# Optimization experiments

Measured on AMD Instinct MI355X. Metric: run time of the kernel, lower is better.

Reference implementation:

```python
import math
import jax, jax.numpy as jnp
import numpy as np

NUM_LAYERS = 2  # init arg num_layers
MASK_FILL = 1e-10  # non-standard fill used by the original (not -inf)


def _pos_encoding(L, D):
    # Matches torch PositionalEncoding buffer (dropout is identity in eval).
    pos = np.arange(L, dtype=np.float32)[:, None]
    div = np.exp(np.arange(0, D, 2, dtype=np.float32) * (-math.log(10000.0) / D))
    pe = np.zeros((L, D), dtype=np.float32)
    pe[:, 0::2] = np.sin(pos * div)
    pe[:, 1::2] = np.cos(pos * div)
    return jnp.asarray(pe)


def setup_inputs() -> dict:
    B, L, D = 1024, 100, 512
    key = jax.random.key(0)
    ks = jax.random.split(key, 6)
    x = jax.random.normal(ks[0], (B, L, D), dtype=jnp.float32)
    text_len = jax.random.randint(ks[1], (B,), 1, L + 1)  # in [1, L]
    scale = 1.0 / np.sqrt(2 * D)  # stand-in for orthogonal init
    W_r = jax.random.normal(ks[2], (2 * D, D), dtype=jnp.float32) * scale
    W_u = jax.random.normal(ks[3], (2 * D, D), dtype=jnp.float32) * scale
    W_o = jax.random.normal(ks[4], (2 * D, D), dtype=jnp.float32) * scale
    b = jnp.zeros((D,), dtype=jnp.float32)
    return {"x": x, "text_len": text_len, "W_r": W_r, "b_r": b,
            "W_u": W_u, "b_u": b, "W_o": W_o, "b_o": b}


def reference(x, text_len, W_r, b_r, W_u, b_u, W_o, b_o):
    B, L, D = x.shape
    pe = _pos_encoding(L, D)  # [L, D]
    valid = jnp.arange(L)[None, :] < text_len[:, None]          # [B, L]
    mask = valid[:, :, None] & valid[:, None, :]                 # [B, L, L]
    for _ in range(NUM_LAYERS):
        xp = x + pe  # PE (dropout identity in eval), applied to both sides
        score = jnp.einsum('bld,bmd->blm', xp, xp)               # [B, L, L]
        score = jnp.where(mask, score, MASK_FILL)
        attn = jax.nn.softmax(score, axis=2)
        message = jnp.einsum('blm,bmd->bld', attn, x)            # [B, L, D]
        # ConvGRU cell (prev_state = x): gates are Linear on last dim
        si = jnp.concatenate([message, x], axis=-1)              # [B, L, 2D]
        update = jax.nn.sigmoid(si @ W_u + b_u)
        reset = jax.nn.sigmoid(si @ W_r + b_r)
        so = jnp.concatenate([message, x * reset], axis=-1)
        cand = jnp.tanh(so @ W_o + b_o)
        x = x * (1.0 - update) + cand * update
    # mean_with_lens pooling
    lenf = text_len.astype(x.dtype)
    seq_emb = jnp.sum(x * valid[:, :, None].astype(x.dtype), axis=1) / lenf[:, None]
    return x, seq_emb
```

## Files before the change

kernel.cpp:

```cpp
#include <hip/hip_runtime.h>
#include <hip/hip_bf16.h>

#define B_ 1024
#define L_ 100
#define D_ 512
#define LP 128
#define ROWS (B_*L_)
#define XELEMS ((size_t)ROWS*D_)
#define HB 512
#define HR (HB*L_)
#define CATW 1536

typedef __attribute__((ext_vector_type(8))) short short8;
typedef __attribute__((ext_vector_type(4))) float f32x4;

__device__ __forceinline__ short f2bf(float f) {
    __hip_bfloat16 h = __float2bfloat16(f);
    return *reinterpret_cast<short*>(&h);
}
__device__ __forceinline__ float bf2f(short s) {
    __hip_bfloat16 h = *reinterpret_cast<__hip_bfloat16*>(&s);
    return __bfloat162float(h);
}

__device__ __forceinline__ void cp16(void* lds, const void* g) {
    __builtin_amdgcn_global_load_lds(
        (const __attribute__((address_space(1))) unsigned int*)g,
        (__attribute__((address_space(3))) unsigned int*)lds, 16, 0, 0);
}

__device__ __forceinline__ f32x4 mfma16(short8 a, short8 b, f32x4 c) {
    return __builtin_amdgcn_mfma_f32_16x16x32_bf16(a, b, c, 0, 0, 0);
}

__global__ __launch_bounds__(256) void pe_kernel(float* __restrict__ pe) {
    int idx = blockIdx.x * 256 + threadIdx.x;
    if (idx >= L_ * D_) return;
    int l = idx >> 9;
    int d = idx & 511;
    int i = d >> 1;
    float div = __expf((float)(2 * i) * (-9.210340371976184f / 512.0f));
    float angle = (float)l * div;
    pe[idx] = (d & 1) ? __cosf(angle) : __sinf(angle);
}

__global__ __launch_bounds__(256) void cvtw_kernel(const float* __restrict__ W,
                                                   __hip_bfloat16* __restrict__ Wt) {
    int idx = blockIdx.x * 256 + threadIdx.x;
    int n = idx >> 10, k = idx & 1023;
    Wt[idx] = __float2bfloat16(W[(size_t)k * D_ + n]);
}

template<int BF16IN>
__global__ __launch_bounds__(256) void prep_xt_kernel(const float* __restrict__ x,
                                                      __hip_bfloat16* __restrict__ xTb,
                                                      __hip_bfloat16* __restrict__ cat,
                                                      int bh) {
    const int bl = blockIdx.y;
    const int b = bh * HB + bl;
    const int d0 = blockIdx.x * 64;
    __shared__ __hip_bfloat16 t[64][66];
    const float* xb = x + (size_t)b * L_ * D_;
    const int tid = threadIdx.x;
    for (int l0 = 0; l0 < LP; l0 += 64) {
        int l_loc = tid >> 2;
        int dq = tid & 3;
        int l = l0 + l_loc;
        #pragma unroll
        for (int i = 0; i < 4; ++i) {
            int d_loc = (dq * 4 + i) * 4;
            if constexpr (BF16IN) {
                unsigned long long u = 0ull;
                if (l < L_)
                    u = *(const unsigned long long*)(cat + ((size_t)bl * L_ + l) * CATW + 512 + d0 + d_loc);
                union { unsigned long long u; short s[4]; } pk;
                pk.u = u;
                t[l_loc][d_loc + 0] = *reinterpret_cast<__hip_bfloat16*>(&pk.s[0]);
                t[l_loc][d_loc + 1] = *reinterpret_cast<__hip_bfloat16*>(&pk.s[1]);
                t[l_loc][d_loc + 2] = *reinterpret_cast<__hip_bfloat16*>(&pk.s[2]);
                t[l_loc][d_loc + 3] = *reinterpret_cast<__hip_bfloat16*>(&pk.s[3]);
            } else {
                float4 v = (l < L_) ? *(const float4*)(xb + (size_t)l * D_ + d0 + d_loc)
                                    : make_float4(0.f, 0.f, 0.f, 0.f);
                short s0 = f2bf(v.x), s1 = f2bf(v.y), s2 = f2bf(v.z), s3 = f2bf(v.w);
                t[l_loc][d_loc + 0] = *reinterpret_cast<__hip_bfloat16*>(&s0);
                t[l_loc][d_loc + 1] = *reinterpret_cast<__hip_bfloat16*>(&s1);
                t[l_loc][d_loc + 2] = *reinterpret_cast<__hip_bfloat16*>(&s2);
                t[l_loc][d_loc + 3] = *reinterpret_cast<__hip_bfloat16*>(&s3);
                if (l < L_) {
                    union { short s[4]; unsigned long long u; } pk;
                    pk.s[0] = s0; pk.s[1] = s1; pk.s[2] = s2; pk.s[3] = s3;
                    *(unsigned long long*)(cat + ((size_t)bl * L_ + l) * CATW + 512 + d0 + d_loc) = pk.u;
                }
            }
        }
        __syncthreads();
        int dl = tid >> 2, seg = tid & 3;
        short8 lo, hi;
        #pragma unroll
        for (int j = 0; j < 8; ++j) {
            __hip_bfloat16 a = t[seg * 16 + j][dl];
            __hip_bfloat16 bswap = t[seg * 16 + 8 + j][dl];
            lo[j] = *reinterpret_cast<short*>(&a);
            hi[j] = *reinterpret_cast<short*>(&bswap);
        }
        __hip_bfloat16* dst = xTb + ((size_t)bl * D_ + d0 + dl) * LP + l0 + seg * 16;
        *(short8*)dst = lo;
        *(short8*)(dst + 8) = hi;
        __syncthreads();
    }
}

template<int BF16IN>
__global__ __launch_bounds__(256) void attn_kernel(
    const float* __restrict__ x, const float* __restrict__ pe,
    const int* __restrict__ text_len, const __hip_bfloat16* __restrict__ xTb,
    __hip_bfloat16* __restrict__ cat, int bh)
{
    __shared__ __align__(16) char sm[16384 + 32768];
    char* XP = sm;
    char* P  = sm + 16384;
    const int bl = blockIdx.x;
    const int b = bh * HB + bl;
    const int len = text_len[b];
    const int tid = threadIdx.x;
    const int w = tid >> 6, g = (tid >> 4) & 3, cl = tid & 15;
    const int lane = tid & 63;
    const float* xb = x + (size_t)b * L_ * D_;

    f32x4 accS[2][8];
    const f32x4 fz = {0.f, 0.f, 0.f, 0.f};
    #pragma unroll
    for (int i = 0; i < 2; ++i)
        #pragma unroll
        for (int j = 0; j < 8; ++j) accS[i][j] = fz;

    for (int kc = 0; kc < D_; kc += 64) {
        #pragma unroll
        for (int i = 0; i < 4; ++i) {
            int c = tid + 256 * i;
            int row = c >> 3, k8d = c & 7;
            int k = kc + 8 * (k8d ^ (row & 7));
            if (row < L_) {
                const float* pp = pe + row * D_ + k;
                float4 b0 = *(const float4*)pp, b1 = *(const float4*)(pp + 4);
                short8 h;
                if constexpr (BF16IN) {
                    short8 xv = *(const short8*)(cat + ((size_t)bl * L_ + row) * CATW + 512 + k);
                    h[0] = f2bf(bf2f(xv[0]) + b0.x); h[1] = f2bf(bf2f(xv[1]) + b0.y);
                    h[2] = f2bf(bf2f(xv[2]) + b0.z); h[3] = f2bf(bf2f(xv[3]) + b0.w);
                    h[4] = f2bf(bf2f(xv[4]) + b1.x); h[5] = f2bf(bf2f(xv[5]) + b1.y);
                    h[6] = f2bf(bf2f(xv[6]) + b1.z); h[7] = f2bf(bf2f(xv[7]) + b1.w);
                } else {
                    const float* px = xb + (size_t)row * D_ + k;
                    float4 a0 = *(const float4*)px, a1 = *(const float4*)(px + 4);
                    h[0] = f2bf(a0.x + b0.x); h[1] = f2bf(a0.y + b0.y);
                    h[2] = f2bf(a0.z + b0.z); h[3] = f2bf(a0.w + b0.w);
                    h[4] = f2bf(a1.x + b1.x); h[5] = f2bf(a1.y + b1.y);
                    h[6] = f2bf(a1.z + b1.z); h[7] = f2bf(a1.w + b1.w);
                }
                *(short8*)(XP + row * 128 + 16 * k8d) = h;
            } else if (kc == 0) {
                short8 h;
                #pragma unroll
                for (int q = 0; q < 8; ++q) h[q] = 0;
                *(short8*)(XP + row * 128 + 16 * k8d) = h;
            }
        }
        __syncthreads();
        #pragma unroll
        for (int kt = 0; kt < 2; ++kt) {
            short8 a[2];
            #pragma unroll
            for (int rt = 0; rt < 2; ++rt) {
                int r = 32 * w + 16 * rt + cl;
                a[rt] = *(const short8*)(XP + r * 128 + ((16 * g + 64 * kt) ^ ((r & 7) << 4)));
            }
            #pragma unroll
            for (int ct = 0; ct < 8; ++ct) {
                int m = 16 * ct + cl;
                short8 bb = *(const short8*)(XP + m * 128 + ((16 * g + 64 * kt) ^ ((m & 7) << 4)));
                accS[0][ct] = mfma16(a[0], bb, accS[0][ct]);
                accS[1][ct] = mfma16(a[1], bb, accS[1][ct]);
            }
        }
        __syncthreads();
    }

    #pragma unroll
    for (int rt = 0; rt < 2; ++rt) {
        #pragma unroll
        for (int reg = 0; reg < 4; ++reg) {
            int rl = 32 * w + 16 * rt + 4 * g + reg;
            float s[8];
            #pragma unroll
            for (int ct = 0; ct < 8; ++ct) {
                int col = 16 * ct + cl;
                float v = accS[rt][ct][reg];
                if (col >= L_) v = -INFINITY;
                else if (rl >= len || col >= len) v = 1e-10f;
                s[ct] = v;
            }
            float mx = s[0];
            #pragma unroll
            for (int ct = 1; ct < 8; ++ct) mx = fmaxf(mx, s[ct]);
            mx = fmaxf(mx, __shfl_xor(mx, 1));
            mx = fmaxf(mx, __shfl_xor(mx, 2));
            mx = fmaxf(mx, __shfl_xor(mx, 4));
            mx = fmaxf(mx, __shfl_xor(mx, 8));
            float e[8], sum = 0.f;
            #pragma unroll
            for (int ct = 0; ct < 8; ++ct) { e[ct] = __expf(s[ct] - mx); sum += e[ct]; }
            sum += __shfl_xor(sum, 1);
            sum += __shfl_xor(sum, 2);
            sum += __shfl_xor(sum, 4);
            sum += __shfl_xor(sum, 8);
            float inv = 1.f / sum;
            #pragma unroll
            for (int ct = 0; ct < 8; ++ct) {
                int col = 16 * ct + cl;
                *(short*)(P + rl * 256 + ((col * 2) ^ ((rl & 7) << 4))) = f2bf(e[ct] * inv);
            }
        }
    }

    const __hip_bfloat16* xT = xTb + (size_t)bl * D_ * LP;
    char* TW = XP + w * 4096;
    for (int nc = 0; nc < 4; ++nc) {
        f32x4 accM[2][8];
        #pragma unroll
        for (int i = 0; i < 2; ++i)
            #pragma unroll
            for (int j = 0; j < 8; ++j) accM[i][j] = fz;
        #pragma unroll
        for (int kt = 0; kt < 4; ++kt) {
            short8 a[2];
            #pragma unroll
            for (int rt = 0; rt < 2; ++rt) {
                int r = 32 * w + 16 * rt + cl;
                a[rt] = *(const short8*)(P + r * 256 + ((16 * g + 64 * kt) ^ ((r & 7) << 4)));
            }
            #pragma unroll
            for (int nt = 0; nt < 8; ++nt) {
                int d = nc * 128 + nt * 16 + cl;
                short8 bb = *(const short8*)(xT + (size_t)d * LP + 8 * g + 32 * kt);
                accM[0][nt] = mfma16(a[0], bb, accM[0][nt]);
                accM[1][nt] = mfma16(a[1], bb, accM[1][nt]);
            }
        }
        #pragma unroll
        for (int rt = 0; rt < 2; ++rt) {
            #pragma unroll
            for (int nt = 0; nt < 8; ++nt) {
                #pragma unroll
                for (int reg = 0; reg < 4; ++reg) {
                    int rloc = 4 * g + reg;
                    int cc = nt * 16 + cl;
                    *(short*)(TW + rloc * 256 + ((2 * cc) ^ ((rloc & 15) << 4))) =
                        f2bf(accM[rt][nt][reg]);
                }
            }
            asm volatile("s_waitcnt lgkmcnt(0)" ::: "memory");
            __builtin_amdgcn_sched_barrier(0);
            int r2 = lane >> 2, cq = lane & 3;
            int rl = 32 * w + 16 * rt + r2;
            if (rl < L_) {
                #pragma unroll
                for (int j2 = 0; j2 < 4; ++j2) {
                    int byte = (cq * 64 + j2 * 16) ^ ((r2 & 15) << 4);
                    short8 v = *(const short8*)(TW + r2 * 256 + byte);
                    int d = nc * 128 + cq * 32 + j2 * 8;
                    *(short8*)(cat + ((size_t)bl * L_ + rl) * CATW + d) = v;
                }
            }
            asm volatile("s_waitcnt lgkmcnt(0)" ::: "memory");
            __builtin_amdgcn_sched_barrier(0);
        }
    }
}

template<int MODE, int LAST>
__global__ __launch_bounds__(256) void gemm_gates(
    const __hip_bfloat16* __restrict__ cat,
    const __hip_bfloat16* __restrict__ Wt,
    const float* __restrict__ bias0, const float* __restrict__ bias1,
    __hip_bfloat16* __restrict__ upd,
    __hip_bfloat16* __restrict__ catw,
    float* __restrict__ xdst)
{
    __shared__ __align__(16) char sm[32768];
    const int tid = threadIdx.x;
    const int w = tid >> 6, g = (tid >> 4) & 3, cl = tid & 15;
    const int wr = w >> 1, wc = w & 1;
    constexpr int NY = (MODE == 0) ? 8 : 4;
    const int cpx = gridDim.x >> 3;
    const int bid = blockIdx.x;
    const int swz = (bid & 7) * cpx + (bid >> 3);
    const int bx = swz / NY, by = swz % NY;
    const size_t R0 = (size_t)bx * 128;
    const int col0 = by * 128;

    int srow[2], skoff[2];
    #pragma unroll
    for (int i = 0; i < 2; ++i) {
        int p = tid + 256 * i;
        int R = p >> 3, s = p & 7;
        int u = s ^ (R & 7);
        srow[i] = 2 * R + (u >> 2);
        skoff[i] = (u & 3) * 16;
    }

    auto stage = [&](int t, char* buf) {
        const int kc = t * 32;
        const int ka = (MODE == 0) ? kc : (t < 16 ? kc : kc + 512);
        #pragma unroll
        for (int i = 0; i < 2; ++i) {
            int p = tid + 256 * i;
            const char* gA = (const char*)(cat + (R0 + srow[i]) * CATW + ka) + skoff[i];
            cp16(buf + p * 16, gA);
        }
        #pragma unroll
        for (int i = 0; i < 2; ++i) {
            int p = tid + 256 * i;
            const char* gB = (const char*)(Wt + (size_t)(col0 + srow[i]) * 1024 + kc) + skoff[i];
            cp16(buf + 8192 + p * 16, gB);
        }
    };

    f32x4 acc[4][4];
    const f32x4 fz = {0.f, 0.f, 0.f, 0.f};
    #pragma unroll
    for (int i = 0; i < 4; ++i)
        #pragma unroll
        for (int j = 0; j < 4; ++j) acc[i][j] = fz;

    stage(0, sm);
    #pragma unroll 1
    for (int t = 0; t < 32; ++t) {
        char* buf = sm + ((t & 1) << 14);
        char* nbuf = sm + (((t + 1) & 1) << 14);
        if (t + 1 < 32) {
            stage(t + 1, nbuf);
            asm volatile("s_waitcnt vmcnt(4)" ::: "memory");
        } else {
            asm volatile("s_waitcnt vmcnt(0)" ::: "memory");
        }
        __builtin_amdgcn_sched_barrier(0);
        __builtin_amdgcn_s_barrier();

        short8 aA[4], bb[4];
        #pragma unroll
        for (int rt = 0; rt < 4; ++rt) {
            int r = wr * 64 + rt * 16 + cl;
            int Rr = r >> 1;
            int sA = (((r & 1) << 2) + g) ^ (Rr & 7);
            aA[rt] = *(const short8*)(buf + Rr * 128 + 16 * sA);
        }
        #pragma unroll
        for (int ct = 0; ct < 4; ++ct) {
            int n = wc * 64 + ct * 16 + cl;
            int Rn = n >> 1;
            int sB = (((n & 1) << 2) + g) ^ (Rn & 7);
            bb[ct] = *(const short8*)(buf + 8192 + Rn * 128 + 16 * sB);
        }
        __builtin_amdgcn_s_setprio(1);
        #pragma unroll
        for (int rt = 0; rt < 4; ++rt)
            #pragma unroll
            for (int ct = 0; ct < 4; ++ct)
                acc[rt][ct] = mfma16(aA[rt], bb[ct], acc[rt][ct]);
        __builtin_amdgcn_s_setprio(0);
        __builtin_amdgcn_s_barrier();
    }

    char* T = sm;
    #pragma unroll
    for (int ct = 0; ct < 4; ++ct) {
        int c = wc * 64 + ct * 16 + cl;
        int colg = col0 + c;
        float bb = (MODE == 0) ? ((col0 < 512) ? bias0[colg] : bias1[colg - 512])
                               : bias0[colg];
        #pragma unroll
        for (int rt = 0; rt < 4; ++rt) {
            #pragma unroll
            for (int reg = 0; reg < 4; ++reg) {
                int r = wr * 64 + rt * 16 + g * 4 + reg;
                float z = acc[rt][ct][reg] + bb;
                float v;
                if (MODE == 0) v = 1.f / (1.f + __expf(-z));
                else           v = 1.f - 2.f * __fdividef(1.f, 1.f + __expf(2.f * z));
                *(short*)(T + r * 256 + ((2 * c) ^ ((r & 15) << 4))) = f2bf(v);
            }
        }
    }
    __syncthreads();
    {
        const int r = tid >> 1, hf = tid & 1;
        const size_t grow = R0 + r;
        #pragma unroll
        for (int j = 0; j < 8; ++j) {
            int byte = (hf * 128 + j * 16) ^ ((r & 15) << 4);
            short8 v = *(const short8*)(T + r * 256 + byte);
            int cloc = hf * 64 + j * 8;
            int colg = col0 + cloc;
            if (MODE == 0) {
                if (col0 < 512) {
                    *(short8*)(upd + grow * D_ + colg) = v;
                } else {
                    int c2 = colg - 512;
                    short8 xv = *(const short8*)(cat + grow * CATW + 512 + c2);
                    short8 o;
                    #pragma unroll
                    for (int q = 0; q < 8; ++q)
                        o[q] = f2bf(bf2f(xv[q]) * bf2f(v[q]));
                    *(short8*)(catw + grow * CATW + 1024 + c2) = o;
                }
            } else {
                short8 uv = *(const short8*)(upd + grow * D_ + colg);
                short8 xv = *(const short8*)(cat + grow * CATW + 512 + colg);
                if (LAST) {
                    float o[8];
                    #pragma unroll
                    for (int q = 0; q < 8; ++q) {
                        float u = bf2f(uv[q]), x_ = bf2f(xv[q]), cd = bf2f(v[q]);
                        o[q] = x_ + u * (cd - x_);
                    }
                    *(float4*)(xdst + grow * D_ + colg)     = make_float4(o[0], o[1], o[2], o[3]);
                    *(float4*)(xdst + grow * D_ + colg + 4) = make_float4(o[4], o[5], o[6], o[7]);
                } else {
                    short8 o;
                    #pragma unroll
                    for (int q = 0; q < 8; ++q) {
                        float u = bf2f(uv[q]), x_ = bf2f(xv[q]), cd = bf2f(v[q]);
                        o[q] = f2bf(x_ + u * (cd - x_));
                    }
                    *(short8*)(catw + grow * CATW + 512 + colg) = o;
                }
            }
        }
    }
}

__global__ __launch_bounds__(256) void pool_kernel(
    const float* __restrict__ x, const int* __restrict__ text_len,
    float* __restrict__ seq)
{
    int b = blockIdx.x;
    int len = text_len[b];
    float invlen = 1.f / (float)len;
    const float* xb = x + (size_t)b * L_ * D_;
    for (int d = threadIdx.x; d < D_; d += 256) {
        float acc = 0.f;
        for (int l = 0; l < len; ++l)
            acc += xb[(size_t)l * D_ + d];
        seq[(size_t)b * D_ + d] = acc * invlen;
    }
}

extern "C" void kernel_launch(void* const* d_in, const int* in_sizes, int n_in,
                              void* d_out, int out_size, void* d_ws, size_t ws_size,
                              hipStream_t stream) {
    const float* x_in = (const float*)d_in[0];
    const int* text_len = (const int*)d_in[1];
    const float* W_r = (const float*)d_in[2];
    const float* b_r = (const float*)d_in[3];
    const float* W_u = (const float*)d_in[4];
    const float* b_u = (const float*)d_in[5];
    const float* W_o = (const float*)d_in[6];
    const float* b_o = (const float*)d_in[7];

    float* xwork = (float*)d_out;
    float* seq_out = (float*)d_out + XELEMS;

    char* ws = (char*)d_ws;
    float* pe            = (float*)ws;
    __hip_bfloat16* WurT = (__hip_bfloat16*)(ws + 204800);
    __hip_bfloat16* WoT  = (__hip_bfloat16*)(ws + 2301952);
    __hip_bfloat16* cat  = (__hip_bfloat16*)(ws + 3350528);
    char* unionR         = ws + 160636928ull;
    __hip_bfloat16* xTb  = (__hip_bfloat16*)unionR;
    __hip_bfloat16* upd  = (__hip_bfloat16*)unionR;

    pe_kernel<<<(L_ * D_ + 255) / 256, 256, 0, stream>>>(pe);
    cvtw_kernel<<<2048, 256, 0, stream>>>(W_u, WurT);
    cvtw_kernel<<<2048, 256, 0, stream>>>(W_r, WurT + 512 * 1024);
    cvtw_kernel<<<2048, 256, 0, stream>>>(W_o, WoT);

    for (int h = 0; h < 2; ++h) {
        float* xdh = xwork + (size_t)h * HR * D_;
        prep_xt_kernel<0><<<dim3(8, HB), 256, 0, stream>>>(x_in, xTb, cat, h);
        attn_kernel<0><<<HB, 256, 0, stream>>>(x_in, pe, text_len, xTb, cat, h);
        gemm_gates<0, 0><<<3200, 256, 0, stream>>>(cat, WurT, b_u, b_r, upd, cat, nullptr);
        gemm_gates<1, 0><<<1600, 256, 0, stream>>>(cat, WoT, b_o, nullptr, upd, cat, nullptr);
        prep_xt_kernel<1><<<dim3(8, HB), 256, 0, stream>>>(nullptr, xTb, cat, h);
        attn_kernel<1><<<HB, 256, 0, stream>>>(nullptr, pe, text_len, xTb, cat, h);
        gemm_gates<0, 0><<<3200, 256, 0, stream>>>(cat, WurT, b_u, b_r, upd, cat, nullptr);
        gemm_gates<1, 1><<<1600, 256, 0, stream>>>(cat, WoT, b_o, nullptr, upd, cat, xdh);
    }
    pool_kernel<<<B_, 256, 0, stream>>>(xwork, text_len, seq_out);
}
```

Measured before the change: 1.792 ms.

## Fuse transpose prep into attention kernel and enlarge gate GEMM tiles

The separate prep_xt kernel that converts x to bf16, writes it into cat and builds the transposed copy is folded into the start of the attention kernel. Each block now does that transpose for its batch element itself, and the QK load then always reads the bf16 x from cat. The gate GEMMs move to 512-thread blocks with 256-row tiles (256 or 128 columns) and a two-pass epilogue through a 64KB LDS buffer, which raises operand reuse and cuts the block count. In exchange the attention kernel gets a serial transpose prologue, and the larger GEMM blocks lower occupancy and may reduce latency hiding.

```diff
diff --git a/kernel.cpp b/kernel.cpp
--- a/kernel.cpp
+++ b/kernel.cpp
@@ -13,6 +13,7 @@
 
 typedef __attribute__((ext_vector_type(8))) short short8;
 typedef __attribute__((ext_vector_type(4))) float f32x4;
+typedef unsigned long long ull_t;
 
 __device__ __forceinline__ short f2bf(float f) {
     __hip_bfloat16 h = __float2bfloat16(f);
@@ -52,69 +53,9 @@
 }
 
 template<int BF16IN>
-__global__ __launch_bounds__(256) void prep_xt_kernel(const float* __restrict__ x,
-                                                      __hip_bfloat16* __restrict__ xTb,
-                                                      __hip_bfloat16* __restrict__ cat,
-                                                      int bh) {
-    const int bl = blockIdx.y;
-    const int b = bh * HB + bl;
-    const int d0 = blockIdx.x * 64;
-    __shared__ __hip_bfloat16 t[64][66];
-    const float* xb = x + (size_t)b * L_ * D_;
-    const int tid = threadIdx.x;
-    for (int l0 = 0; l0 < LP; l0 += 64) {
-        int l_loc = tid >> 2;
-        int dq = tid & 3;
-        int l = l0 + l_loc;
-        #pragma unroll
-        for (int i = 0; i < 4; ++i) {
-            int d_loc = (dq * 4 + i) * 4;
-            if constexpr (BF16IN) {
-                unsigned long long u = 0ull;
-                if (l < L_)
-                    u = *(const unsigned long long*)(cat + ((size_t)bl * L_ + l) * CATW + 512 + d0 + d_loc);
-                union { unsigned long long u; short s[4]; } pk;
-                pk.u = u;
-                t[l_loc][d_loc + 0] = *reinterpret_cast<__hip_bfloat16*>(&pk.s[0]);
-                t[l_loc][d_loc + 1] = *reinterpret_cast<__hip_bfloat16*>(&pk.s[1]);
-                t[l_loc][d_loc + 2] = *reinterpret_cast<__hip_bfloat16*>(&pk.s[2]);
-                t[l_loc][d_loc + 3] = *reinterpret_cast<__hip_bfloat16*>(&pk.s[3]);
-            } else {
-                float4 v = (l < L_) ? *(const float4*)(xb + (size_t)l * D_ + d0 + d_loc)
-                                    : make_float4(0.f, 0.f, 0.f, 0.f);
-                short s0 = f2bf(v.x), s1 = f2bf(v.y), s2 = f2bf(v.z), s3 = f2bf(v.w);
-                t[l_loc][d_loc + 0] = *reinterpret_cast<__hip_bfloat16*>(&s0);
-                t[l_loc][d_loc + 1] = *reinterpret_cast<__hip_bfloat16*>(&s1);
-                t[l_loc][d_loc + 2] = *reinterpret_cast<__hip_bfloat16*>(&s2);
-                t[l_loc][d_loc + 3] = *reinterpret_cast<__hip_bfloat16*>(&s3);
-                if (l < L_) {
-                    union { short s[4]; unsigned long long u; } pk;
-                    pk.s[0] = s0; pk.s[1] = s1; pk.s[2] = s2; pk.s[3] = s3;
-                    *(unsigned long long*)(cat + ((size_t)bl * L_ + l) * CATW + 512 + d0 + d_loc) = pk.u;
-                }
-            }
-        }
-        __syncthreads();
-        int dl = tid >> 2, seg = tid & 3;
-        short8 lo, hi;
-        #pragma unroll
-        for (int j = 0; j < 8; ++j) {
-            __hip_bfloat16 a = t[seg * 16 + j][dl];
-            __hip_bfloat16 bswap = t[seg * 16 + 8 + j][dl];
-            lo[j] = *reinterpret_cast<short*>(&a);
-            hi[j] = *reinterpret_cast<short*>(&bswap);
-        }
-        __hip_bfloat16* dst = xTb + ((size_t)bl * D_ + d0 + dl) * LP + l0 + seg * 16;
-        *(short8*)dst = lo;
-        *(short8*)(dst + 8) = hi;
-        __syncthreads();
-    }
-}
-
-template<int BF16IN>
 __global__ __launch_bounds__(256) void attn_kernel(
     const float* __restrict__ x, const float* __restrict__ pe,
-    const int* __restrict__ text_len, const __hip_bfloat16* __restrict__ xTb,
+    const int* __restrict__ text_len, __hip_bfloat16* __restrict__ xTb,
     __hip_bfloat16* __restrict__ cat, int bh)
 {
     __shared__ __align__(16) char sm[16384 + 32768];
@@ -127,6 +68,60 @@
     const int w = tid >> 6, g = (tid >> 4) & 3, cl = tid & 15;
     const int lane = tid & 63;
     const float* xb = x + (size_t)b * L_ * D_;
+    __hip_bfloat16* xTg = xTb + (size_t)bl * D_ * LP;
+
+    {
+        __hip_bfloat16 (*t)[66] = (__hip_bfloat16 (*)[66])XP;
+        for (int d0 = 0; d0 < D_; d0 += 64) {
+            for (int l0 = 0; l0 < LP; l0 += 64) {
+                int l_loc = tid >> 2;
+                int dq = tid & 3;
+                int l = l0 + l_loc;
+                #pragma unroll
+                for (int i = 0; i < 4; ++i) {
+                    int d_loc = (dq * 4 + i) * 4;
+                    if constexpr (BF16IN) {
+                        ull_t u = 0ull;
+                        if (l < L_)
+                            u = *(const ull_t*)(cat + ((size_t)bl * L_ + l) * CATW + 512 + d0 + d_loc);
+                        union { ull_t u; short s[4]; } pk;
+                        pk.u = u;
+                        t[l_loc][d_loc + 0] = *reinterpret_cast<__hip_bfloat16*>(&pk.s[0]);
+                        t[l_loc][d_loc + 1] = *reinterpret_cast<__hip_bfloat16*>(&pk.s[1]);
+                        t[l_loc][d_loc + 2] = *reinterpret_cast<__hip_bfloat16*>(&pk.s[2]);
+                        t[l_loc][d_loc + 3] = *reinterpret_cast<__hip_bfloat16*>(&pk.s[3]);
+                    } else {
+                        float4 v = (l < L_) ? *(const float4*)(xb + (size_t)l * D_ + d0 + d_loc)
+                                            : make_float4(0.f, 0.f, 0.f, 0.f);
+                        short s0 = f2bf(v.x), s1 = f2bf(v.y), s2 = f2bf(v.z), s3 = f2bf(v.w);
+                        t[l_loc][d_loc + 0] = *reinterpret_cast<__hip_bfloat16*>(&s0);
+                        t[l_loc][d_loc + 1] = *reinterpret_cast<__hip_bfloat16*>(&s1);
+                        t[l_loc][d_loc + 2] = *reinterpret_cast<__hip_bfloat16*>(&s2);
+                        t[l_loc][d_loc + 3] = *reinterpret_cast<__hip_bfloat16*>(&s3);
+                        if (l < L_) {
+                            union { short s[4]; ull_t u; } pk;
+                            pk.s[0] = s0; pk.s[1] = s1; pk.s[2] = s2; pk.s[3] = s3;
+                            *(ull_t*)(cat + ((size_t)bl * L_ + l) * CATW + 512 + d0 + d_loc) = pk.u;
+                        }
+                    }
+                }
+                __syncthreads();
+                int dl = tid >> 2, seg = tid & 3;
+                short8 lo, hi;
+                #pragma unroll
+                for (int j = 0; j < 8; ++j) {
+                    __hip_bfloat16 a = t[seg * 16 + j][dl];
+                    __hip_bfloat16 bswap = t[seg * 16 + 8 + j][dl];
+                    lo[j] = *reinterpret_cast<short*>(&a);
+                    hi[j] = *reinterpret_cast<short*>(&bswap);
+                }
+                __hip_bfloat16* dst = xTg + (size_t)(d0 + dl) * LP + l0 + seg * 16;
+                *(short8*)dst = lo;
+                *(short8*)(dst + 8) = hi;
+                __syncthreads();
+            }
+        }
+    }
 
     f32x4 accS[2][8];
     const f32x4 fz = {0.f, 0.f, 0.f, 0.f};
@@ -144,21 +139,12 @@
             if (row < L_) {
                 const float* pp = pe + row * D_ + k;
                 float4 b0 = *(const float4*)pp, b1 = *(const float4*)(pp + 4);
+                short8 xv = *(const short8*)(cat + ((size_t)bl * L_ + row) * CATW + 512 + k);
                 short8 h;
-                if constexpr (BF16IN) {
-                    short8 xv = *(const short8*)(cat + ((size_t)bl * L_ + row) * CATW + 512 + k);
-                    h[0] = f2bf(bf2f(xv[0]) + b0.x); h[1] = f2bf(bf2f(xv[1]) + b0.y);
-                    h[2] = f2bf(bf2f(xv[2]) + b0.z); h[3] = f2bf(bf2f(xv[3]) + b0.w);
-                    h[4] = f2bf(bf2f(xv[4]) + b1.x); h[5] = f2bf(bf2f(xv[5]) + b1.y);
-                    h[6] = f2bf(bf2f(xv[6]) + b1.z); h[7] = f2bf(bf2f(xv[7]) + b1.w);
-                } else {
-                    const float* px = xb + (size_t)row * D_ + k;
-                    float4 a0 = *(const float4*)px, a1 = *(const float4*)(px + 4);
-                    h[0] = f2bf(a0.x + b0.x); h[1] = f2bf(a0.y + b0.y);
-                    h[2] = f2bf(a0.z + b0.z); h[3] = f2bf(a0.w + b0.w);
-                    h[4] = f2bf(a1.x + b1.x); h[5] = f2bf(a1.y + b1.y);
-                    h[6] = f2bf(a1.z + b1.z); h[7] = f2bf(a1.w + b1.w);
-                }
+                h[0] = f2bf(bf2f(xv[0]) + b0.x); h[1] = f2bf(bf2f(xv[1]) + b0.y);
+                h[2] = f2bf(bf2f(xv[2]) + b0.z); h[3] = f2bf(bf2f(xv[3]) + b0.w);
+                h[4] = f2bf(bf2f(xv[4]) + b1.x); h[5] = f2bf(bf2f(xv[5]) + b1.y);
+                h[6] = f2bf(bf2f(xv[6]) + b1.z); h[7] = f2bf(bf2f(xv[7]) + b1.w);
                 *(short8*)(XP + row * 128 + 16 * k8d) = h;
             } else if (kc == 0) {
                 short8 h;
@@ -224,7 +210,7 @@
         }
     }
 
-    const __hip_bfloat16* xT = xTb + (size_t)bl * D_ * LP;
+    const __hip_bfloat16* xT = xTg;
     char* TW = XP + w * 4096;
     for (int nc = 0; nc < 4; ++nc) {
         f32x4 accM[2][8];
@@ -280,7 +266,7 @@
 }
 
 template<int MODE, int LAST>
-__global__ __launch_bounds__(256) void gemm_gates(
+__global__ __launch_bounds__(512, 1) void gemm_gates(
     const __hip_bfloat16* __restrict__ cat,
     const __hip_bfloat16* __restrict__ Wt,
     const float* __restrict__ bias0, const float* __restrict__ bias1,
@@ -288,22 +274,25 @@
     __hip_bfloat16* __restrict__ catw,
     float* __restrict__ xdst)
 {
-    __shared__ __align__(16) char sm[32768];
+    constexpr int TN    = MODE ? 128 : 256;
+    constexpr int RT    = MODE ? 4 : 8;
+    constexpr int TILEB = MODE ? 24576 : 32768;
+    __shared__ __align__(16) char sm[65536];
     const int tid = threadIdx.x;
     const int w = tid >> 6, g = (tid >> 4) & 3, cl = tid & 15;
-    const int wr = w >> 1, wc = w & 1;
-    constexpr int NY = (MODE == 0) ? 8 : 4;
+    const int wr = MODE ? (w >> 1) : (w >> 2);
+    const int wc = MODE ? (w & 1) : (w & 3);
     const int cpx = gridDim.x >> 3;
     const int bid = blockIdx.x;
     const int swz = (bid & 7) * cpx + (bid >> 3);
-    const int bx = swz / NY, by = swz % NY;
-    const size_t R0 = (size_t)bx * 128;
-    const int col0 = by * 128;
+    const int bx = swz >> 2, by = swz & 3;
+    const size_t R0 = (size_t)bx * 256;
+    const int col0 = by * TN;
 
     int srow[2], skoff[2];
     #pragma unroll
     for (int i = 0; i < 2; ++i) {
-        int p = tid + 256 * i;
+        int p = tid + 512 * i;
         int R = p >> 3, s = p & 7;
         int u = s ^ (R & 7);
         srow[i] = 2 * R + (u >> 2);
@@ -315,43 +304,48 @@
         const int ka = (MODE == 0) ? kc : (t < 16 ? kc : kc + 512);
         #pragma unroll
         for (int i = 0; i < 2; ++i) {
-            int p = tid + 256 * i;
+            int p = tid + 512 * i;
             const char* gA = (const char*)(cat + (R0 + srow[i]) * CATW + ka) + skoff[i];
             cp16(buf + p * 16, gA);
         }
-        #pragma unroll
-        for (int i = 0; i < 2; ++i) {
-            int p = tid + 256 * i;
-            const char* gB = (const char*)(Wt + (size_t)(col0 + srow[i]) * 1024 + kc) + skoff[i];
-            cp16(buf + 8192 + p * 16, gB);
+        if constexpr (MODE == 0) {
+            #pragma unroll
+            for (int i = 0; i < 2; ++i) {
+                int p = tid + 512 * i;
+                const char* gB = (const char*)(Wt + (size_t)(col0 + srow[i]) * 1024 + kc) + skoff[i];
+                cp16(buf + 16384 + p * 16, gB);
+            }
+        } else {
+            const char* gB = (const char*)(Wt + (size_t)(col0 + srow[0]) * 1024 + kc) + skoff[0];
+            cp16(buf + 16384 + tid * 16, gB);
         }
     };
 
-    f32x4 acc[4][4];
+    f32x4 acc[RT][4];
     const f32x4 fz = {0.f, 0.f, 0.f, 0.f};
     #pragma unroll
-    for (int i = 0; i < 4; ++i)
+    for (int i = 0; i < RT; ++i)
         #pragma unroll
         for (int j = 0; j < 4; ++j) acc[i][j] = fz;
 
     stage(0, sm);
     #pragma unroll 1
     for (int t = 0; t < 32; ++t) {
-        char* buf = sm + ((t & 1) << 14);
-        char* nbuf = sm + (((t + 1) & 1) << 14);
+        char* buf = sm + (t & 1) * TILEB;
         if (t + 1 < 32) {
-            stage(t + 1, nbuf);
-            asm volatile("s_waitcnt vmcnt(4)" ::: "memory");
+            stage(t + 1, sm + ((t + 1) & 1) * TILEB);
+            if constexpr (MODE == 0) asm volatile("s_waitcnt vmcnt(4)" ::: "memory");
+            else                     asm volatile("s_waitcnt vmcnt(3)" ::: "memory");
         } else {
             asm volatile("s_waitcnt vmcnt(0)" ::: "memory");
         }
         __builtin_amdgcn_sched_barrier(0);
         __builtin_amdgcn_s_barrier();
 
-        short8 aA[4], bb[4];
-        #pragma unroll
-        for (int rt = 0; rt < 4; ++rt) {
-            int r = wr * 64 + rt * 16 + cl;
+        short8 aA[RT], bb[4];
+        #pragma unroll
+        for (int rt = 0; rt < RT; ++rt) {
+            int r = wr * (RT * 16) + rt * 16 + cl;
             int Rr = r >> 1;
             int sA = (((r & 1) << 2) + g) ^ (Rr & 7);
             aA[rt] = *(const short8*)(buf + Rr * 128 + 16 * sA);
@@ -361,11 +355,11 @@
             int n = wc * 64 + ct * 16 + cl;
             int Rn = n >> 1;
             int sB = (((n & 1) << 2) + g) ^ (Rn & 7);
-            bb[ct] = *(const short8*)(buf + 8192 + Rn * 128 + 16 * sB);
+            bb[ct] = *(const short8*)(buf + 16384 + Rn * 128 + 16 * sB);
         }
         __builtin_amdgcn_s_setprio(1);
         #pragma unroll
-        for (int rt = 0; rt < 4; ++rt)
+        for (int rt = 0; rt < RT; ++rt)
             #pragma unroll
             for (int ct = 0; ct < 4; ++ct)
                 acc[rt][ct] = mfma16(aA[rt], bb[ct], acc[rt][ct]);
@@ -373,68 +367,77 @@
         __builtin_amdgcn_s_barrier();
     }
 
+    constexpr int TRB = TN * 2;
     char* T = sm;
+    const int rowoff = MODE ? ((wr & 1) * 64) : 0;
     #pragma unroll
-    for (int ct = 0; ct < 4; ++ct) {
-        int c = wc * 64 + ct * 16 + cl;
-        int colg = col0 + c;
-        float bb = (MODE == 0) ? ((col0 < 512) ? bias0[colg] : bias1[colg - 512])
-                               : bias0[colg];
-        #pragma unroll
-        for (int rt = 0; rt < 4; ++rt) {
-            #pragma unroll
-            for (int reg = 0; reg < 4; ++reg) {
-                int r = wr * 64 + rt * 16 + g * 4 + reg;
-                float z = acc[rt][ct][reg] + bb;
-                float v;
-                if (MODE == 0) v = 1.f / (1.f + __expf(-z));
-                else           v = 1.f - 2.f * __fdividef(1.f, 1.f + __expf(2.f * z));
-                *(short*)(T + r * 256 + ((2 * c) ^ ((r & 15) << 4))) = f2bf(v);
-            }
-        }
-    }
-    __syncthreads();
-    {
-        const int r = tid >> 1, hf = tid & 1;
-        const size_t grow = R0 + r;
-        #pragma unroll
-        for (int j = 0; j < 8; ++j) {
-            int byte = (hf * 128 + j * 16) ^ ((r & 15) << 4);
-            short8 v = *(const short8*)(T + r * 256 + byte);
-            int cloc = hf * 64 + j * 8;
-            int colg = col0 + cloc;
-            if (MODE == 0) {
-                if (col0 < 512) {
-                    *(short8*)(upd + grow * D_ + colg) = v;
+    for (int p2 = 0; p2 < 2; ++p2) {
+        __syncthreads();
+        const bool owner = MODE ? ((wr >> 1) == p2) : (wr == p2);
+        if (owner) {
+            #pragma unroll
+            for (int ct = 0; ct < 4; ++ct) {
+                int c = wc * 64 + ct * 16 + cl;
+                int colg = col0 + c;
+                float bb = (MODE == 0) ? ((col0 < 512) ? bias0[colg] : bias1[colg - 512])
+                                       : bias0[colg];
+                #pragma unroll
+                for (int rt = 0; rt < RT; ++rt) {
+                    #pragma unroll
+                    for (int reg = 0; reg < 4; ++reg) {
+                        int rl = rowoff + rt * 16 + g * 4 + reg;
+                        float z = acc[rt][ct][reg] + bb;
+                        float v;
+                        if (MODE == 0) v = 1.f / (1.f + __expf(-z));
+                        else           v = 1.f - 2.f * __fdividef(1.f, 1.f + __expf(2.f * z));
+                        *(short*)(T + rl * TRB + ((2 * c) ^ ((rl & 15) << 4))) = f2bf(v);
+                    }
+                }
+            }
+        }
+        __syncthreads();
+        {
+            const int r = tid >> 2, q = tid & 3;
+            const size_t grow = R0 + p2 * 128 + r;
+            #pragma unroll
+            for (int j = 0; j < TN / 32; ++j) {
+                int byte = (q * (TN / 2) + j * 16) ^ ((r & 15) << 4);
+                short8 v = *(const short8*)(T + r * TRB + byte);
+                int cloc = q * (TN / 4) + j * 8;
+                int colg = col0 + cloc;
+                if (MODE == 0) {
+                    if (col0 < 512) {
+                        *(short8*)(upd + grow * D_ + colg) = v;
+                    } else {
+                        int c2 = colg - 512;
+                        short8 xv = *(const short8*)(cat + grow * CATW + 512 + c2);
+                        short8 o;
+                        #pragma unroll
+                        for (int q2 = 0; q2 < 8; ++q2)
+                            o[q2] = f2bf(bf2f(xv[q2]) * bf2f(v[q2]));
+                        *(short8*)(catw + grow * CATW + 1024 + c2) = o;
+                    }
                 } else {
-                    int c2 = colg - 512;
-                    short8 xv = *(const short8*)(cat + grow * CATW + 512 + c2);
-                    short8 o;
-                    #pragma unroll
-                    for (int q = 0; q < 8; ++q)
-                        o[q] = f2bf(bf2f(xv[q]) * bf2f(v[q]));
-                    *(short8*)(catw + grow * CATW + 1024 + c2) = o;
-                }
-            } else {
-                short8 uv = *(const short8*)(upd + grow * D_ + colg);
-                short8 xv = *(const short8*)(cat + grow * CATW + 512 + colg);
-                if (LAST) {
-                    float o[8];
-                    #pragma unroll
-                    for (int q = 0; q < 8; ++q) {
-                        float u = bf2f(uv[q]), x_ = bf2f(xv[q]), cd = bf2f(v[q]);
-                        o[q] = x_ + u * (cd - x_);
+                    short8 uv = *(const short8*)(upd + grow * D_ + colg);
+                    short8 xv = *(const short8*)(cat + grow * CATW + 512 + colg);
+                    if (LAST) {
+                        float o[8];
+                        #pragma unroll
+                        for (int q2 = 0; q2 < 8; ++q2) {
+                            float u = bf2f(uv[q2]), x_ = bf2f(xv[q2]), cd = bf2f(v[q2]);
+                            o[q2] = x_ + u * (cd - x_);
+                        }
+                        *(float4*)(xdst + grow * D_ + colg)     = make_float4(o[0], o[1], o[2], o[3]);
+                        *(float4*)(xdst + grow * D_ + colg + 4) = make_float4(o[4], o[5], o[6], o[7]);
+                    } else {
+                        short8 o;
+                        #pragma unroll
+                        for (int q2 = 0; q2 < 8; ++q2) {
+                            float u = bf2f(uv[q2]), x_ = bf2f(xv[q2]), cd = bf2f(v[q2]);
+                            o[q2] = f2bf(x_ + u * (cd - x_));
+                        }
+                        *(short8*)(catw + grow * CATW + 512 + colg) = o;
                     }
-                    *(float4*)(xdst + grow * D_ + colg)     = make_float4(o[0], o[1], o[2], o[3]);
-                    *(float4*)(xdst + grow * D_ + colg + 4) = make_float4(o[4], o[5], o[6], o[7]);
-                } else {
-                    short8 o;
-                    #pragma unroll
-                    for (int q = 0; q < 8; ++q) {
-                        float u = bf2f(uv[q]), x_ = bf2f(xv[q]), cd = bf2f(v[q]);
-                        o[q] = f2bf(x_ + u * (cd - x_));
-                    }
-                    *(short8*)(catw + grow * CATW + 512 + colg) = o;
                 }
             }
         }
@@ -488,14 +491,12 @@
 
     for (int h = 0; h < 2; ++h) {
         float* xdh = xwork + (size_t)h * HR * D_;
-        prep_xt_kernel<0><<<dim3(8, HB), 256, 0, stream>>>(x_in, xTb, cat, h);
         attn_kernel<0><<<HB, 256, 0, stream>>>(x_in, pe, text_len, xTb, cat, h);
-        gemm_gates<0, 0><<<3200, 256, 0, stream>>>(cat, WurT, b_u, b_r, upd, cat, nullptr);
-        gemm_gates<1, 0><<<1600, 256, 0, stream>>>(cat, WoT, b_o, nullptr, upd, cat, nullptr);
-        prep_xt_kernel<1><<<dim3(8, HB), 256, 0, stream>>>(nullptr, xTb, cat, h);
+        gemm_gates<0, 0><<<800, 512, 0, stream>>>(cat, WurT, b_u, b_r, upd, cat, nullptr);
+        gemm_gates<1, 0><<<800, 512, 0, stream>>>(cat, WoT, b_o, nullptr, upd, cat, nullptr);
         attn_kernel<1><<<HB, 256, 0, stream>>>(nullptr, pe, text_len, xTb, cat, h);
-        gemm_gates<0, 0><<<3200, 256, 0, stream>>>(cat, WurT, b_u, b_r, upd, cat, nullptr);
-        gemm_gates<1, 1><<<1600, 256, 0, stream>>>(cat, WoT, b_o, nullptr, upd, cat, xdh);
+        gemm_gates<0, 0><<<800, 512, 0, stream>>>(cat, WurT, b_u, b_r, upd, cat, nullptr);
+        gemm_gates<1, 1><<<800, 512, 0, stream>>>(cat, WoT, b_o, nullptr, upd, cat, xdh);
     }
     pool_kernel<<<B_, 256, 0, stream>>>(xwork, text_len, seq_out);
 }
```

New measurement: 1.823 ms. Within noise of the previous version (+1.7%).
